# Optimization experiments

Measured on AMD Instinct MI355X. Metric: run time of the kernel, lower is better.

## Reference

```python
import jax, jax.numpy as jnp
import numpy as np

H = 16        # num_attention_heads
KV = 4        # num_key_value_heads
DH = 128      # head_dim
THETA = 10000.0
MIN_VAL = -1000000000000000.0


def _rope_tables(L):
    # inv_freq: (DH/2,), positions: (L,)
    inv_freq = 1.0 / (THETA ** (jnp.arange(0, DH, 2, dtype=jnp.float32) / DH))
    pos = jnp.arange(L, dtype=jnp.float32)
    freq = pos[:, None] * inv_freq[None, :]          # (L, DH/2)
    emb = jnp.concatenate([freq, freq], axis=-1)      # (L, DH)
    return jnp.cos(emb), jnp.sin(emb)


def _apply_rope(x, cos, sin):
    # x: (B, h, L, DH); cos/sin: (L, DH)
    left = x[..., : DH // 2]
    right = -x[..., DH // 2 :]
    rot = jnp.concatenate([right, left], axis=-1)
    return x * cos[None, None] + rot * sin[None, None]


def setup_inputs() -> dict:
    key = jax.random.key(0)
    ks = jax.random.split(key, 5)
    B, L, D = 2, 2048, 2048
    s = 0.02
    return {
        "hidden_state": jax.random.normal(ks[0], (B, L, D), jnp.float32),
        "attention_mask": jnp.ones((B, L), jnp.int32),
        "Wq": jax.random.normal(ks[1], (H * DH, D), jnp.float32) * s,
        "Wk": jax.random.normal(ks[2], (KV * DH, D), jnp.float32) * s,
        "Wv": jax.random.normal(ks[3], (KV * DH, D), jnp.float32) * s,
        "Wo": jax.random.normal(ks[4], (D, D), jnp.float32) * s,
    }


def reference(hidden_state, attention_mask, Wq, Wk, Wv, Wo):
    B, L, D = hidden_state.shape
    cos, sin = _rope_tables(L)

    q = jnp.einsum('bld,ed->ble', hidden_state, Wq).reshape(B, L, H, DH).transpose(0, 2, 1, 3)
    k = jnp.einsum('bld,ed->ble', hidden_state, Wk).reshape(B, L, KV, DH).transpose(0, 2, 1, 3)
    v = jnp.einsum('bld,ed->ble', hidden_state, Wv).reshape(B, L, KV, DH).transpose(0, 2, 1, 3)

    q = _apply_rope(q, cos, sin)
    k = _apply_rope(k, cos, sin)

    # GQA: repeat each KV head H/KV times -> (B, H, L, DH)
    g = H // KV
    k = jnp.repeat(k, g, axis=1)
    v = jnp.repeat(v, g, axis=1)

    scores = jnp.einsum('bhqd,bhkd->bhqk', q, k) / np.sqrt(DH)  # (B,H,L,L)

    causal = jnp.triu(jnp.full((L, L), MIN_VAL, jnp.float32), k=1)[None, None]  # (1,1,L,L)
    pad = (attention_mask == 0)[:, None, None, :]  # (B,1,1,L)
    mask = jnp.where(pad, MIN_VAL, causal)
    scores = scores + mask

    attn = jax.nn.softmax(scores.astype(jnp.float32), axis=-1).astype(q.dtype)
    out = jnp.einsum('bhqk,bhkd->bhqd', attn, v)
    out = out.transpose(0, 2, 1, 3).reshape(B, L, H * DH)
    return jnp.einsum('ble,de->bld', out, Wo)
```

## Files before the change

kernel.cpp:

```cpp
#include <hip/hip_runtime.h>
#include <cstdint>
#include <cmath>


typedef __bf16 bf16_t;
typedef __bf16 bf16x8 __attribute__((ext_vector_type(8)));
typedef __bf16 bf16x4 __attribute__((ext_vector_type(4)));
typedef float  f32x4  __attribute__((ext_vector_type(4)));

#define HQ   16
#define HKV  4
#define GQA  4
#define DHD  128
#define BB   2
#define LL   2048
#define DDIM 2048
#define MINV (-1e15f)
#define QSC  0.12751744f

static __device__ __forceinline__ f32x4 mfma16(bf16x8 a, bf16x8 b, f32x4 c) {
  return __builtin_amdgcn_mfma_f32_16x16x32_bf16(a, b, c, 0, 0, 0);
}

static __device__ __forceinline__ f32x4 mfma16k16(bf16x4 a, bf16x4 b, f32x4 c) {
#if __has_builtin(__builtin_amdgcn_mfma_f32_16x16x16bf16_1k)
  typedef short s4 __attribute__((ext_vector_type(4)));
  union U { bf16x4 h; s4 s; };
  U ua, ub; ua.h = a; ub.h = b;
  return __builtin_amdgcn_mfma_f32_16x16x16bf16_1k(ua.s, ub.s, c, 0, 0, 0);
#elif __has_builtin(__builtin_amdgcn_mfma_f32_16x16x16_bf16)
  return __builtin_amdgcn_mfma_f32_16x16x16_bf16(a, b, c, 0, 0, 0);
#else
  f32x4 d;
  asm volatile("v_mfma_f32_16x16x16_bf16 %0, %1, %2, %3"
               : "=v"(d) : "v"(a), "v"(b), "v"(c));
  return d;
#endif
}

#if __has_builtin(__builtin_amdgcn_exp2f)
#define EXP2F(x) __builtin_amdgcn_exp2f(x)
#else
#define EXP2F(x) exp2f(x)
#endif

static __device__ __forceinline__ void gld16(const bf16_t* g, bf16_t* l) {
  __builtin_amdgcn_global_load_lds(
      (const __attribute__((address_space(1))) void*)g,
      (__attribute__((address_space(3))) void*)l,
      16, 0, 0);
}

struct CastArgs {
  const float* s[5];
  bf16_t* d[5];
  int n[5];
};

__global__ __launch_bounds__(256) void cast5_kernel(CastArgs a) {
  const int t = blockIdx.y;
  const int i8 = (blockIdx.x * 256 + threadIdx.x) * 8;
  if (i8 >= a.n[t]) return;
  const float4* s = (const float4*)(a.s[t] + i8);
  float4 x = s[0], y = s[1];
  bf16x8 o = {(bf16_t)x.x, (bf16_t)x.y, (bf16_t)x.z, (bf16_t)x.w,
              (bf16_t)y.x, (bf16_t)y.y, (bf16_t)y.z, (bf16_t)y.w};
  *(bf16x8*)(a.d[t] + i8) = o;
}

template <int STORE>
__global__ __launch_bounds__(256) void gemm_tile(const bf16_t* __restrict__ A,
                                                 const bf16_t* __restrict__ W,
                                                 void* __restrict__ C0,
                                                 bf16_t* __restrict__ Ck,
                                                 bf16_t* __restrict__ Cv,
                                                 int M, int N, int K) {
  __shared__ __align__(16) bf16_t As[128 * 32];
  __shared__ __align__(16) bf16_t Bs[128 * 32];
  const int tid  = threadIdx.x;
  const int lane = tid & 63;
  const int wave = tid >> 6;
  const int l15  = lane & 15;
  const int quad = lane >> 4;
  const int m0 = blockIdx.y * 128;
  const int n0 = blockIdx.x * 128;

  const int srow = wave * 32 + (lane >> 2);
  const int scol = (lane & 3) * 8;
  const bf16_t* ag = A + (size_t)(m0 + srow) * K + scol;
  const bf16_t* wg = W + (size_t)(n0 + srow) * K + scol;
  bf16_t* al = As + wave * 1024;
  bf16_t* bl = Bs + wave * 1024;

  const int wm = (wave >> 1) * 64;
  const int wn = (wave & 1) * 64;

  f32x4 acc[4][4];
#pragma unroll
  for (int mi = 0; mi < 4; mi++)
#pragma unroll
    for (int ni = 0; ni < 4; ni++) acc[mi][ni] = {0.f, 0.f, 0.f, 0.f};

  for (int k0 = 0; k0 < K; k0 += 32) {
    __syncthreads();
    gld16(ag + k0, al);
    gld16(ag + k0 + (size_t)16 * K, al + 512);
    gld16(wg + k0, bl);
    gld16(wg + k0 + (size_t)16 * K, bl + 512);
    __syncthreads();
    bf16x8 af[4], bfr[4];
#pragma unroll
    for (int mi = 0; mi < 4; mi++)
      af[mi] = *(const bf16x8*)(As + (wm + mi * 16 + l15) * 32 + quad * 8);
#pragma unroll
    for (int ni = 0; ni < 4; ni++)
      bfr[ni] = *(const bf16x8*)(Bs + (wn + ni * 16 + l15) * 32 + quad * 8);
#pragma unroll
    for (int mi = 0; mi < 4; mi++)
#pragma unroll
      for (int ni = 0; ni < 4; ni++)
        acc[mi][ni] = mfma16(af[mi], bfr[ni], acc[mi][ni]);
  }

  if (STORE == 2) {
    float* C = (float*)C0;
#pragma unroll
    for (int mi = 0; mi < 4; mi++) {
      const int row = m0 + wm + mi * 16 + quad * 4;
#pragma unroll
      for (int ni = 0; ni < 4; ni++) {
        const int col = n0 + wn + ni * 16 + l15;
#pragma unroll
        for (int i = 0; i < 4; i++)
          C[(size_t)(row + i) * N + col] = acc[mi][ni][i];
      }
    }
  } else {
    if (n0 < 2048) {
      bf16_t* C = (bf16_t*)C0;
#pragma unroll
      for (int mi = 0; mi < 4; mi++) {
        const int row = m0 + wm + mi * 16 + quad * 4;
#pragma unroll
        for (int ni = 0; ni < 4; ni++) {
          const int col = n0 + wn + ni * 16 + l15;
#pragma unroll
          for (int i = 0; i < 4; i++)
            C[(size_t)(row + i) * 2048 + col] = (bf16_t)acc[mi][ni][i];
        }
      }
    } else if (n0 < 2560) {
#pragma unroll
      for (int mi = 0; mi < 4; mi++) {
        const int row = m0 + wm + mi * 16 + quad * 4;
#pragma unroll
        for (int ni = 0; ni < 4; ni++) {
          const int col = n0 - 2048 + wn + ni * 16 + l15;
#pragma unroll
          for (int i = 0; i < 4; i++)
            Ck[(size_t)(row + i) * 512 + col] = (bf16_t)acc[mi][ni][i];
        }
      }
    } else {
#pragma unroll
      for (int mi = 0; mi < 4; mi++) {
        const int row = m0 + wm + mi * 16 + quad * 4;
        const int b = row >> 11;
        const int l0 = row & (LL - 1);
#pragma unroll
        for (int ni = 0; ni < 4; ni++) {
          const int kvcol = n0 - 2560 + wn + ni * 16 + l15;
          const int kvh = kvcol >> 7, d = kvcol & 127;
          bf16x4 w4 = {(bf16_t)acc[mi][ni][0], (bf16_t)acc[mi][ni][1],
                       (bf16_t)acc[mi][ni][2], (bf16_t)acc[mi][ni][3]};
          *(bf16x4*)(Cv + ((size_t)(b * HKV + kvh) * DHD + d) * LL + l0) = w4;
        }
      }
    }
  }
}

__global__ void rope_kernel(bf16_t* __restrict__ q, bf16_t* __restrict__ k,
                            const int* __restrict__ amask, float* __restrict__ bias) {
  const int nq = BB * LL * HQ * 64;
  const int nk = BB * LL * HKV * 64;
  int id = blockIdx.x * blockDim.x + threadIdx.x;
  if (id >= nq + nk) {
    int id2 = id - (nq + nk);
    if (id2 < BB * LL) bias[id2] = (amask[id2] == 0) ? MINV : 0.0f;
    return;
  }
  bf16_t* base;
  int heads, idx;
  float sc;
  if (id < nq) { base = q; heads = HQ; idx = id; sc = QSC; }
  else         { base = k; heads = HKV; idx = id - nq; sc = 1.0f; }
  int d = idx & 63; idx >>= 6;
  int hh = idx % heads;
  int bl = idx / heads;
  int l = bl & (LL - 1);
  bf16_t* p = base + ((size_t)bl * heads + hh) * DHD + d;
  float x1 = (float)p[0];
  float x2 = (float)p[64];
  float invf = __expf(-(float)d * 0.14391156862532788f);
  float fr = (float)l * invf;
  float s, c;
  __sincosf(fr, &s, &c);
  p[0]  = (bf16_t)((x1 * c - x2 * s) * sc);
  p[64] = (bf16_t)((x2 * c + x1 * s) * sc);
}

__global__ __launch_bounds__(512, 4) void flash_attn2(const bf16_t* __restrict__ q,
                                                      const bf16_t* __restrict__ k,
                                                      const bf16_t* __restrict__ vt,
                                                      const float* __restrict__ bias,
                                                      bf16_t* __restrict__ o) {
  __shared__ __align__(16) bf16_t Kbuf[2][64 * 128];
  __shared__ __align__(16) bf16_t Vbuf[2][128 * 64];
  __shared__ __align__(16) float  Bb[2048];

  const int tid  = threadIdx.x;
  const int lane = tid & 63;
  const int wave = tid >> 6;
  const int l15  = lane & 15;
  const int quad = lane >> 4;

  const int bi   = blockIdx.x;
  const int half = bi >> 8;
  const int jj   = bi & 255;
  const int cc   = jj >> 5;
  const int c    = half ? (15 - cc) : cc;
  const int bh = jj & 31;
  const int b  = bh >> 4;
  const int h  = bh & 15;
  const int kv = h >> 2;

  const int tile = (wave < 4) ? c : (31 - c);
  const int q0   = tile * 64 + (wave & 3) * 16;
  const int nrounds = 32 - c;

  bf16x8 qf[4];
  {
    const bf16_t* qb = q + ((size_t)(b * LL + q0 + l15)) * (HQ * DHD) + h * DHD + quad * 8;
#pragma unroll
    for (int t = 0; t < 4; t++) qf[t] = *(const bf16x8*)(qb + 32 * t);
  }

  f32x4 acc[8];
#pragma unroll
  for (int mt = 0; mt < 8; mt++) acc[mt] = {0.f, 0.f, 0.f, 0.f};
  float m_i = -1e30f;
  float l_i = 0.f;

  const bf16_t* kg_base = k + ((size_t)(b * LL)) * (HKV * DHD) + kv * DHD;
  const bf16_t* vg_base = vt + ((size_t)(b * HKV + kv) * DHD) * LL;
  const float*  bias_b  = bias + b * LL;

  ((float4*)Bb)[tid] = ((const float4*)bias_b)[tid];

  const int krow = tid >> 4, kch = tid & 15;
  const int vrow = tid >> 3, vch = tid & 7;
  const int vc0  = ((vch >> 2) << 5) + (((vch << 1) & 3) << 3) + (((vch >> 1) & 1) << 2);
  const int vblo = vc0 * 2;
  const int ksw  = (krow & 7) << 4;
  const int vsw  = (vrow & 7) << 4;
  const int rsw  = (l15 & 7) << 4;

  const bf16_t* kg0 = kg_base + (size_t)krow * (HKV * DHD) + kch * 8;
  const bf16_t* vg0 = vg_base + (size_t)vrow * LL + vch * 8;

  bf16x8 kl[2], vl[2];
  auto ISSUE = [&](int j0) {
#pragma unroll
    for (int p = 0; p < 2; p++)
      kl[p] = *(const bf16x8*)(kg0 + (size_t)(j0 + p * 32) * (HKV * DHD));
#pragma unroll
    for (int p = 0; p < 2; p++)
      vl[p] = *(const bf16x8*)(vg0 + j0 + (size_t)p * 64 * LL);
  };
  auto STAGE = [&](int bsel) {
    char* kb = (char*)(&Kbuf[bsel][0]);
    char* vb = (char*)(&Vbuf[bsel][0]);
#pragma unroll
    for (int p = 0; p < 2; p++)
      *(bf16x8*)(kb + (size_t)(krow + p * 32) * 256 + ((kch * 16) ^ ksw)) = kl[p];
#pragma unroll
    for (int p = 0; p < 2; p++) {
      char* vbase = vb + (size_t)(vrow + p * 64) * 128;
      bf16x4 lo4 = __builtin_shufflevector(vl[p], vl[p], 0, 1, 2, 3);
      bf16x4 hi4 = __builtin_shufflevector(vl[p], vl[p], 4, 5, 6, 7);
      *(bf16x4*)(vbase + (vblo ^ vsw)) = lo4;
      *(bf16x4*)(vbase + ((vblo + 16) ^ vsw)) = hi4;
    }
  };

  ISSUE(0);
  STAGE(0);
  __syncthreads();

  int cur = 0;
  for (int r = 0; r < nrounds; r++) {
    const int j0 = r * 64;
    const bool last = (r + 1 >= nrounds);
    if (!last) ISSUE(j0 + 64);

    const bool act = (j0 <= q0 + 15);
    if (act) {
      const char* KbC = (const char*)(&Kbuf[cur][0]);
      const char* VbC = (const char*)(&Vbuf[cur][0]);

      f32x4 s[4];
      __builtin_amdgcn_s_setprio(1);
#pragma unroll
      for (int kt = 0; kt < 4; kt++) {
        const char* kr = KbC + (size_t)(kt * 16 + l15) * 256;
        f32x4 s0 = {0.f, 0.f, 0.f, 0.f};
#pragma unroll
        for (int t = 0; t < 4; t++) {
          bf16x8 kf = *(const bf16x8*)(kr + ((quad * 16 + t * 64) ^ rsw));
          s0 = mfma16(kf, qf[t], s0);
        }
        s[kt] = s0;
      }
      __builtin_amdgcn_s_setprio(0);

      const int qrow = q0 + l15;
      const bool diag = (j0 + 63 > q0);
      float mx = -1e30f;
#pragma unroll
      for (int kt = 0; kt < 4; kt++) {
        f32x4 sv = s[kt];
        f32x4 bv = *(const f32x4*)(&Bb[j0 + kt * 16 + quad * 4]);
#pragma unroll
        for (int i = 0; i < 4; i++) {
          float x = sv[i] + bv[i];
          if (diag) {
            int key = j0 + kt * 16 + quad * 4 + i;
            if (key > qrow) x = MINV;
          }
          sv[i] = x;
          mx = fmaxf(mx, x);
        }
        s[kt] = sv;
      }
      if (!__all(mx <= m_i + 8.0f)) {
        mx = fmaxf(mx, __shfl_xor(mx, 16));
        mx = fmaxf(mx, __shfl_xor(mx, 32));
        const float mn = fmaxf(m_i, mx);
        const float alpha = EXP2F(m_i - mn);
        m_i = mn;
        l_i *= alpha;
#pragma unroll
        for (int mt = 0; mt < 8; mt++) {
          acc[mt][0] *= alpha; acc[mt][1] *= alpha;
          acc[mt][2] *= alpha; acc[mt][3] *= alpha;
        }
      }
      const float mn = m_i;
      float sum = 0.f;
      bf16x4 pf[4];
#pragma unroll
      for (int kt = 0; kt < 4; kt++) {
        f32x4 sv = s[kt];
        bf16x4 p4;
#pragma unroll
        for (int i = 0; i < 4; i++) {
          float pe = EXP2F(sv[i] - mn);
          sum += pe;
          p4[i] = (bf16_t)pe;
        }
        pf[kt] = p4;
      }
      l_i += sum;

      __builtin_amdgcn_s_setprio(1);
#pragma unroll
      for (int mt = 0; mt < 8; mt++) {
        const char* vr = VbC + (size_t)(mt * 16 + l15) * 128;
        bf16x8 v01 = *(const bf16x8*)(vr + ((quad * 16) ^ rsw));
        bf16x8 v23 = *(const bf16x8*)(vr + ((64 + quad * 16) ^ rsw));
        bf16x4 va = __builtin_shufflevector(v01, v01, 0, 1, 2, 3);
        bf16x4 vb = __builtin_shufflevector(v01, v01, 4, 5, 6, 7);
        bf16x4 vc = __builtin_shufflevector(v23, v23, 0, 1, 2, 3);
        bf16x4 vd = __builtin_shufflevector(v23, v23, 4, 5, 6, 7);
        acc[mt] = mfma16k16(va, pf[0], acc[mt]);
        acc[mt] = mfma16k16(vb, pf[1], acc[mt]);
        acc[mt] = mfma16k16(vc, pf[2], acc[mt]);
        acc[mt] = mfma16k16(vd, pf[3], acc[mt]);
      }
      __builtin_amdgcn_s_setprio(0);
    }

    if (!last) {
      STAGE(cur ^ 1);
      __syncthreads();
      cur ^= 1;
    }
  }

  {
    l_i += __shfl_xor(l_i, 16);
    l_i += __shfl_xor(l_i, 32);
    const float invl = 1.0f / l_i;
    bf16_t* ob = o + ((size_t)(b * LL + q0 + l15)) * (HQ * DHD) + h * DHD + quad * 4;
#pragma unroll
    for (int mt = 0; mt < 8; mt++) {
      f32x4 a = acc[mt];
      bf16x4 w = {(bf16_t)(a[0] * invl), (bf16_t)(a[1] * invl),
                  (bf16_t)(a[2] * invl), (bf16_t)(a[3] * invl)};
      *(bf16x4*)(ob + mt * 16) = w;
    }
  }
}

extern "C" void kernel_launch(void* const* d_in, const int* in_sizes, int n_in,
                              void* d_out, int out_size, void* d_ws, size_t ws_size,
                              hipStream_t stream) {
  const float* hidden = (const float*)d_in[0];
  const int*   amask  = (const int*)d_in[1];
  const float* Wq     = (const float*)d_in[2];
  const float* Wk     = (const float*)d_in[3];
  const float* Wv     = (const float*)d_in[4];
  const float* Wo     = (const float*)d_in[5];
  float* out = (float*)d_out;

  const int M = BB * LL;
  const size_t MB = 1u << 20;
  char* ws = (char*)d_ws;
  bf16_t* hid_b   = (bf16_t*)(ws);
  bf16_t* q_ws    = (bf16_t*)(ws + 16 * MB);
  bf16_t* attn_ws = (bf16_t*)(ws + 32 * MB);
  bf16_t* k_ws    = (bf16_t*)(ws + 48 * MB);
  bf16_t* vt_ws   = (bf16_t*)(ws + 52 * MB);
  bf16_t* wqkv_b  = (bf16_t*)(ws + 56 * MB);
  bf16_t* wq_b    = wqkv_b;
  bf16_t* wk_b    = (bf16_t*)(ws + 64 * MB);
  bf16_t* wv_b    = (bf16_t*)(ws + 66 * MB);
  bf16_t* wo_b    = (bf16_t*)(ws + 68 * MB);
  float*  bias_ws = (float*)(ws);

  CastArgs ca;
  ca.s[0] = hidden; ca.d[0] = hid_b; ca.n[0] = BB * LL * DDIM;
  ca.s[1] = Wq;     ca.d[1] = wq_b;  ca.n[1] = HQ * DHD * DDIM;
  ca.s[2] = Wk;     ca.d[2] = wk_b;  ca.n[2] = HKV * DHD * DDIM;
  ca.s[3] = Wv;     ca.d[3] = wv_b;  ca.n[3] = HKV * DHD * DDIM;
  ca.s[4] = Wo;     ca.d[4] = wo_b;  ca.n[4] = DDIM * DDIM;
  {
    int maxn = BB * LL * DDIM;
    dim3 g((maxn / 8 + 255) / 256, 5);
    cast5_kernel<<<g, 256, 0, stream>>>(ca);
  }

  gemm_tile<3><<<dim3(3072 / 128, M / 128), 256, 0, stream>>>(
      hid_b, wqkv_b, q_ws, k_ws, vt_ws, M, 3072, DDIM);

  {
    int total = BB * LL * (HQ + HKV) * 64 + BB * LL;
    rope_kernel<<<(total + 255) / 256, 256, 0, stream>>>(q_ws, k_ws, amask, bias_ws);
  }

  flash_attn2<<<512, 512, 0, stream>>>(q_ws, k_ws, vt_ws, bias_ws, attn_ws);

  gemm_tile<2><<<dim3(DDIM / 128, M / 128), 256, 0, stream>>>(
      attn_ws, wo_b, (void*)out, nullptr, nullptr, M, DDIM, DDIM);
}
```

Before: 308.5 us.

## Fuse RoPE into QKV GEMM epilogue and build mask bias inside attention

Moves the rotary embedding into the QKV projection's epilogue. Wave pairs exchange their accumulator halves through shared memory so each lane holds both partners of a rotation pair, and Q is pre-scaled before the bf16 store. The padding bias is now built from the int mask directly in the attention kernel. Together these remove the separate RoPE/bias kernel, one launch, and a read-modify-write pass over Q and K. The cost is extra LDS, block barriers, and sincos work in the GEMM epilogue, plus rounding RoPE from fp32 accumulators instead of already-rounded bf16 values.

```diff
diff --git a/kernel.cpp b/kernel.cpp
--- a/kernel.cpp
+++ b/kernel.cpp
@@ -77,6 +77,7 @@
                                                  int M, int N, int K) {
   __shared__ __align__(16) bf16_t As[128 * 32];
   __shared__ __align__(16) bf16_t Bs[128 * 32];
+  __shared__ float Ex[(STORE == 3) ? (4 * 16 * 128) : 4];
   const int tid  = threadIdx.x;
   const int lane = tid & 63;
   const int wave = tid >> 6;
@@ -136,29 +137,42 @@
       }
     }
   } else {
-    if (n0 < 2048) {
-      bf16_t* C = (bf16_t*)C0;
+    if (n0 < 2560) {
+      const bool isq = (n0 < 2048);
+      const int pair = wave >> 1;
+      float* exw = Ex + (pair * 16 + quad * 4) * 128 + wn + l15;
+      const float* exr = Ex + (pair * 16 + quad * 4) * 128 + (wn ^ 64) + l15;
 #pragma unroll
       for (int mi = 0; mi < 4; mi++) {
+        __syncthreads();
+#pragma unroll
+        for (int ni = 0; ni < 4; ni++)
+#pragma unroll
+          for (int i = 0; i < 4; i++)
+            exw[i * 128 + ni * 16] = acc[mi][ni][i];
+        __syncthreads();
         const int row = m0 + wm + mi * 16 + quad * 4;
 #pragma unroll
         for (int ni = 0; ni < 4; ni++) {
-          const int col = n0 + wn + ni * 16 + l15;
-#pragma unroll
-          for (int i = 0; i < 4; i++)
-            C[(size_t)(row + i) * 2048 + col] = (bf16_t)acc[mi][ni][i];
-        }
-      }
-    } else if (n0 < 2560) {
-#pragma unroll
-      for (int mi = 0; mi < 4; mi++) {
-        const int row = m0 + wm + mi * 16 + quad * 4;
-#pragma unroll
-        for (int ni = 0; ni < 4; ni++) {
-          const int col = n0 - 2048 + wn + ni * 16 + l15;
-#pragma unroll
-          for (int i = 0; i < 4; i++)
-            Ck[(size_t)(row + i) * 512 + col] = (bf16_t)acc[mi][ni][i];
+          const int dl = ni * 16 + l15;
+          const float invf = __expf(-(float)dl * 0.14391156862532788f);
+#pragma unroll
+          for (int i = 0; i < 4; i++) {
+            const int l = (row + i) & (LL - 1);
+            float sn, cs;
+            __sincosf((float)l * invf, &sn, &cs);
+            const float own = acc[mi][ni][i];
+            const float oth = exr[i * 128 + ni * 16];
+            const float out = (wn == 0) ? (own * cs - oth * sn)
+                                        : (own * cs + oth * sn);
+            if (isq) {
+              ((bf16_t*)C0)[(size_t)(row + i) * 2048 + (n0 + wn + dl)] =
+                  (bf16_t)(out * QSC);
+            } else {
+              Ck[(size_t)(row + i) * 512 + (n0 - 2048 + wn + dl)] =
+                  (bf16_t)out;
+            }
+          }
         }
       }
     } else {
@@ -180,40 +194,10 @@
   }
 }
 
-__global__ void rope_kernel(bf16_t* __restrict__ q, bf16_t* __restrict__ k,
-                            const int* __restrict__ amask, float* __restrict__ bias) {
-  const int nq = BB * LL * HQ * 64;
-  const int nk = BB * LL * HKV * 64;
-  int id = blockIdx.x * blockDim.x + threadIdx.x;
-  if (id >= nq + nk) {
-    int id2 = id - (nq + nk);
-    if (id2 < BB * LL) bias[id2] = (amask[id2] == 0) ? MINV : 0.0f;
-    return;
-  }
-  bf16_t* base;
-  int heads, idx;
-  float sc;
-  if (id < nq) { base = q; heads = HQ; idx = id; sc = QSC; }
-  else         { base = k; heads = HKV; idx = id - nq; sc = 1.0f; }
-  int d = idx & 63; idx >>= 6;
-  int hh = idx % heads;
-  int bl = idx / heads;
-  int l = bl & (LL - 1);
-  bf16_t* p = base + ((size_t)bl * heads + hh) * DHD + d;
-  float x1 = (float)p[0];
-  float x2 = (float)p[64];
-  float invf = __expf(-(float)d * 0.14391156862532788f);
-  float fr = (float)l * invf;
-  float s, c;
-  __sincosf(fr, &s, &c);
-  p[0]  = (bf16_t)((x1 * c - x2 * s) * sc);
-  p[64] = (bf16_t)((x2 * c + x1 * s) * sc);
-}
-
 __global__ __launch_bounds__(512, 4) void flash_attn2(const bf16_t* __restrict__ q,
                                                       const bf16_t* __restrict__ k,
                                                       const bf16_t* __restrict__ vt,
-                                                      const float* __restrict__ bias,
+                                                      const int* __restrict__ amask,
                                                       bf16_t* __restrict__ o) {
   __shared__ __align__(16) bf16_t Kbuf[2][64 * 128];
   __shared__ __align__(16) bf16_t Vbuf[2][128 * 64];
@@ -254,9 +238,13 @@
 
   const bf16_t* kg_base = k + ((size_t)(b * LL)) * (HKV * DHD) + kv * DHD;
   const bf16_t* vg_base = vt + ((size_t)(b * HKV + kv) * DHD) * LL;
-  const float*  bias_b  = bias + b * LL;
-
-  ((float4*)Bb)[tid] = ((const float4*)bias_b)[tid];
+
+  {
+    int4 am = ((const int4*)(amask + b * LL))[tid];
+    f32x4 bv = { am.x ? 0.f : MINV, am.y ? 0.f : MINV,
+                 am.z ? 0.f : MINV, am.w ? 0.f : MINV };
+    ((f32x4*)Bb)[tid] = bv;
+  }
 
   const int krow = tid >> 4, kch = tid & 15;
   const int vrow = tid >> 3, vch = tid & 7;
@@ -437,7 +425,6 @@
   bf16_t* wk_b    = (bf16_t*)(ws + 64 * MB);
   bf16_t* wv_b    = (bf16_t*)(ws + 66 * MB);
   bf16_t* wo_b    = (bf16_t*)(ws + 68 * MB);
-  float*  bias_ws = (float*)(ws);
 
   CastArgs ca;
   ca.s[0] = hidden; ca.d[0] = hid_b; ca.n[0] = BB * LL * DDIM;
@@ -454,12 +441,7 @@
   gemm_tile<3><<<dim3(3072 / 128, M / 128), 256, 0, stream>>>(
       hid_b, wqkv_b, q_ws, k_ws, vt_ws, M, 3072, DDIM);
 
-  {
-    int total = BB * LL * (HQ + HKV) * 64 + BB * LL;
-    rope_kernel<<<(total + 255) / 256, 256, 0, stream>>>(q_ws, k_ws, amask, bias_ws);
-  }
-
-  flash_attn2<<<512, 512, 0, stream>>>(q_ws, k_ws, vt_ws, bias_ws, attn_ws);
+  flash_attn2<<<512, 512, 0, stream>>>(q_ws, k_ws, vt_ws, amask, attn_ws);
 
   gemm_tile<2><<<dim3(DDIM / 128, M / 128), 256, 0, stream>>>(
       attn_ws, wo_b, (void*)out, nullptr, nullptr, M, DDIM, DDIM);
```

Measured after the change: 307.1 us. Within noise of the previous version (-0.4%).
